# Kernel tuning notes

Hardware: AMD Instinct MI355X
Metric: run time of the kernel (lower is better)

Reference implementation:

```python
import jax, jax.numpy as jnp
import numpy as np

HEAD_NUM = 8
NEG_BIG = 1e9  # additive mask constant from the original layer


def setup_inputs() -> dict:
    key = jax.random.key(0)
    ks = jax.random.split(key, 7)
    B, S, D = 4, 2048, 512
    return {
        "x": jax.random.normal(ks[0], (B, S, D), dtype=jnp.float32),
        "Wk": jax.random.normal(ks[1], (D, D), dtype=jnp.float32) * (1.0 / np.sqrt(D)),
        "bk": jax.random.normal(ks[2], (D,), dtype=jnp.float32) * 0.02,
        "Wv": jax.random.normal(ks[3], (D, D), dtype=jnp.float32) * (1.0 / np.sqrt(D)),
        "bv": jax.random.normal(ks[4], (D,), dtype=jnp.float32) * 0.02,
        "Wo": jax.random.normal(ks[5], (D, D), dtype=jnp.float32) * (1.0 / np.sqrt(D)),
        "bo": jax.random.normal(ks[6], (D,), dtype=jnp.float32) * 0.02,
    }


def reference(x, Wk, bk, Wv, bv, Wo, bo):
    B, S, D = x.shape
    H = HEAD_NUM
    hd = D // H
    # Original layer: query is NOT projected; key/value are.
    q = x
    k = x @ Wk + bk
    v = x @ Wv + bv
    # split heads: [B, H, S, hd]
    qh = q.reshape(B, S, H, hd).transpose(0, 2, 1, 3)
    kh = k.reshape(B, S, H, hd).transpose(0, 2, 1, 3)
    vh = v.reshape(B, S, H, hd).transpose(0, 2, 1, 3)
    # scaled dot-product scores [B, H, S, S] (normalized=True => 1/sqrt(head_dim))
    scale = 1.0 / jnp.sqrt(jnp.asarray(hd, dtype=x.dtype))
    e = jnp.einsum("bhqd,bhkd->bhqk", qh, kh) * scale
    # history_only=True => causal additive mask
    causal = jnp.tril(jnp.ones((S, S), dtype=x.dtype))
    e = e - (1.0 - causal) * NEG_BIG
    a = jax.nn.softmax(e, axis=-1)
    out = jnp.einsum("bhqk,bhkd->bhqd", a, vh)  # [B, H, S, hd]
    out = out.transpose(0, 2, 1, 3).reshape(B, S, D)
    return out @ Wo + bo
```

## Files before the change

kernel.cpp:

```cpp
#include <hip/hip_runtime.h>
#include <stdint.h>
#include <stddef.h>

typedef short bf16x8 __attribute__((ext_vector_type(8)));
typedef float f32x4 __attribute__((ext_vector_type(4)));
typedef int i32x4 __attribute__((ext_vector_type(4)));

#define AS1 __attribute__((address_space(1)))
#define AS3 __attribute__((address_space(3)))

#define KSCALE 0.18033688011112042f

__device__ __forceinline__ unsigned short f2bf(float f) {
    union { float f; uint32_t u; } v; v.f = f;
    return (unsigned short)((v.u + 0x7fffu + ((v.u >> 16) & 1u)) >> 16);
}

__global__ void cvt_f32_bf16(const float* __restrict__ in, unsigned short* __restrict__ out, int n4) {
    int i = blockIdx.x * blockDim.x + threadIdx.x;
    if (i >= n4) return;
    float4 v = reinterpret_cast<const float4*>(in)[i];
    ushort4 o;
    o.x = f2bf(v.x); o.y = f2bf(v.y); o.z = f2bf(v.z); o.w = f2bf(v.w);
    reinterpret_cast<ushort4*>(out)[i] = o;
}

__global__ void wtrans3(const float* __restrict__ Wk, const float* __restrict__ Wv,
                        const float* __restrict__ Wo,
                        unsigned short* __restrict__ WkT, unsigned short* __restrict__ WvT,
                        unsigned short* __restrict__ WoT) {
    __shared__ float tile[32][33];
    const float* W = (blockIdx.z == 0) ? Wk : (blockIdx.z == 1) ? Wv : Wo;
    unsigned short* WT = (blockIdx.z == 0) ? WkT : (blockIdx.z == 1) ? WvT : WoT;
    int bk = blockIdx.x * 32, bn = blockIdx.y * 32;
    int tx = threadIdx.x, ty = threadIdx.y;
#pragma unroll
    for (int r = 0; r < 32; r += 8)
        tile[ty + r][tx] = W[(size_t)(bk + ty + r) * 512 + bn + tx];
    __syncthreads();
#pragma unroll
    for (int r = 0; r < 32; r += 8)
        WT[(size_t)(bn + ty + r) * 512 + bk + tx] = f2bf(tile[tx][ty + r]);
}

template<int EPI>
__global__ __launch_bounds__(256, 2) void gemm64(const unsigned short* __restrict__ A,
                                                 const unsigned short* __restrict__ BT,
                                                 const float* __restrict__ bias,
                                                 void* __restrict__ outp) {
    __shared__ unsigned short lA[64 * 64];
    __shared__ unsigned short lB[128 * 64];
    const int tid = threadIdx.x;
    const int tile_n = blockIdx.x * 128;
    const int tile_m = blockIdx.y * 64;
    const int wid = tid >> 6, lane = tid & 63;
    const int wm = (wid >> 1) * 32, wn = (wid & 1) * 64;
    const int l16 = lane & 15, lg = lane >> 4;

    f32x4 acc[2][4];
#pragma unroll
    for (int i = 0; i < 2; ++i)
#pragma unroll
        for (int j = 0; j < 4; ++j)
            acc[i][j] = (f32x4){0.f, 0.f, 0.f, 0.f};

    const int r0 = tid >> 3;
    const int cr = tid & 7;

    for (int kt = 0; kt < 512; kt += 64) {
#pragma unroll
        for (int i = 0; i < 2; ++i) {
            int r = r0 + i * 32;
            int crs = cr ^ (r & 7);
            __builtin_amdgcn_global_load_lds((const AS1 void*)(A + (size_t)(tile_m + r) * 512 + kt + crs * 8),
                                             (AS3 void*)(&lA[(i * 256 + tid) * 8]), 16, 0, 0);
        }
#pragma unroll
        for (int i = 0; i < 4; ++i) {
            int r = r0 + i * 32;
            int crs = cr ^ (r & 7);
            __builtin_amdgcn_global_load_lds((const AS1 void*)(BT + (size_t)(tile_n + r) * 512 + kt + crs * 8),
                                             (AS3 void*)(&lB[(i * 256 + tid) * 8]), 16, 0, 0);
        }
        __syncthreads();
#pragma unroll
        for (int ks = 0; ks < 2; ++ks) {
            bf16x8 af[2], bfr[4];
#pragma unroll
            for (int f = 0; f < 2; ++f) {
                int ra = wm + f * 16 + l16;
                af[f] = *reinterpret_cast<const bf16x8*>(
                    reinterpret_cast<const char*>(lA) + ra * 128 + (((ks * 4 + lg) ^ (ra & 7)) << 4));
            }
#pragma unroll
            for (int f = 0; f < 4; ++f) {
                int rb = wn + f * 16 + l16;
                bfr[f] = *reinterpret_cast<const bf16x8*>(
                    reinterpret_cast<const char*>(lB) + rb * 128 + (((ks * 4 + lg) ^ (rb & 7)) << 4));
            }
#pragma unroll
            for (int fm = 0; fm < 2; ++fm)
#pragma unroll
                for (int fn = 0; fn < 4; ++fn)
                    acc[fm][fn] = __builtin_amdgcn_mfma_f32_16x16x32_bf16(af[fm], bfr[fn], acc[fm][fn], 0, 0, 0);
        }
        __syncthreads();
    }

#pragma unroll
    for (int fm = 0; fm < 2; ++fm)
#pragma unroll
        for (int fn = 0; fn < 4; ++fn) {
            int gm0 = tile_m + wm + fm * 16 + lg * 4;
            int gn = tile_n + wn + fn * 16 + l16;
            float bs = bias[gn];
#pragma unroll
            for (int r = 0; r < 4; ++r) {
                float v = acc[fm][fn][r] + bs;
                int m = gm0 + r;
                if (EPI == 0) {
                    v *= KSCALE;
                    int b = m >> 11, s = m & 2047, h = gn >> 6, d = gn & 63;
                    ((unsigned short*)outp)[(((size_t)(b * 8 + h) * 2048 + s) << 6) + d] = f2bf(v);
                } else if (EPI == 1) {
                    int b = m >> 11, s = m & 2047, h = gn >> 6, d = gn & 63;
                    ((unsigned short*)outp)[(((size_t)(b * 8 + h) * 64 + d) << 11) + s] = f2bf(v);
                } else {
                    ((float*)outp)[(size_t)m * 512 + gn] = v;
                }
            }
        }
}

__global__ __launch_bounds__(256, 4) void attn_f(const unsigned short* __restrict__ xq,
                                                 const unsigned short* __restrict__ kg,
                                                 const unsigned short* __restrict__ vT,
                                                 unsigned short* __restrict__ ob) {
    __shared__ unsigned short lsK[2][4096];
    __shared__ unsigned short lsV[2][4096];

    const int tid = threadIdx.x;
    const int lane = tid & 63;
    const int w = tid >> 6;
    const int l16 = lane & 15, lg = lane >> 4;
    const int bh = blockIdx.x, b = bh >> 3, h = bh & 7;
    const int qblk = 31 - blockIdx.y;
    const int qlo = qblk * 64 + w * 16;
    const int q = qlo + l16;

    const unsigned short* Kb = kg + (size_t)bh * (2048 * 64);
    const unsigned short* Vb = vT + (size_t)bh * (64 * 2048);

    const unsigned short* qp = xq + ((size_t)(b * 2048 + qlo + l16) * 512) + h * 64 + lg * 8;
    bf16x8 qf0 = *(const bf16x8*)qp;
    bf16x8 qf1 = *(const bf16x8*)(qp + 32);

    f32x4 o[4];
#pragma unroll
    for (int i = 0; i < 4; ++i) o[i] = (f32x4){0.f, 0.f, 0.f, 0.f};
    float lsum = 0.f;

    const int nph = qblk + 1;

    const int srow = tid >> 3;
    const int scs = (tid & 7) ^ (srow & 7);
    const int skey = 8 * ((srow >> 2) & 3) + (srow & 3) + 4 * (srow >> 4);

#define STAGE(B, PH) { \
        const int kv0_ = (PH) << 6; \
        __builtin_amdgcn_global_load_lds((const AS1 void*)(Kb + (size_t)(kv0_ + skey) * 64 + scs * 8), \
            (AS3 void*)(&lsK[B][(size_t)tid * 8]), 16, 0, 0); \
        __builtin_amdgcn_global_load_lds((const AS1 void*)(Kb + (size_t)(kv0_ + 32 + skey) * 64 + scs * 8), \
            (AS3 void*)(&lsK[B][(size_t)(256 + tid) * 8]), 16, 0, 0); \
        __builtin_amdgcn_global_load_lds((const AS1 void*)(Vb + (size_t)srow * 2048 + kv0_ + scs * 8), \
            (AS3 void*)(&lsV[B][(size_t)tid * 8]), 16, 0, 0); \
        __builtin_amdgcn_global_load_lds((const AS1 void*)(Vb + (size_t)(srow + 32) * 2048 + kv0_ + scs * 8), \
            (AS3 void*)(&lsV[B][(size_t)(256 + tid) * 8]), 16, 0, 0); }

#define QKGRP(G, PA, PB, KS, KVB) { \
            const char* r0p = (KS) + (32 * (G) + l16) * 128; \
            const char* r1p = r0p + 16 * 128; \
            bf16x8 k00 = *(const bf16x8*)(r0p + ((lg ^ sw) << 4)); \
            bf16x8 k01 = *(const bf16x8*)(r0p + (((lg + 4) ^ sw) << 4)); \
            bf16x8 k10 = *(const bf16x8*)(r1p + ((lg ^ sw) << 4)); \
            bf16x8 k11 = *(const bf16x8*)(r1p + (((lg + 4) ^ sw) << 4)); \
            f32x4 sA = (f32x4){0.f,0.f,0.f,0.f}, sB = (f32x4){0.f,0.f,0.f,0.f}; \
            __builtin_amdgcn_s_setprio(1); \
            sA = __builtin_amdgcn_mfma_f32_16x16x32_bf16(k00, qf0, sA, 0, 0, 0); \
            sA = __builtin_amdgcn_mfma_f32_16x16x32_bf16(k01, qf1, sA, 0, 0, 0); \
            sB = __builtin_amdgcn_mfma_f32_16x16x32_bf16(k10, qf0, sB, 0, 0, 0); \
            sB = __builtin_amdgcn_mfma_f32_16x16x32_bf16(k11, qf1, sB, 0, 0, 0); \
            __builtin_amdgcn_s_setprio(0); \
            if ((KVB) + 32 * (G) + 31 > qlo) { \
                _Pragma("unroll") \
                for (int r = 0; r < 4; ++r) { \
                    int kidx = (KVB) + 32 * (G) + 8 * lg + r; \
                    PA[r] = __builtin_amdgcn_exp2f(kidx > q ? -1e30f : sA[r]); \
                    PB[r] = __builtin_amdgcn_exp2f(kidx + 4 > q ? -1e30f : sB[r]); \
                } \
            } else { \
                _Pragma("unroll") \
                for (int r = 0; r < 4; ++r) { \
                    PA[r] = __builtin_amdgcn_exp2f(sA[r]); \
                    PB[r] = __builtin_amdgcn_exp2f(sB[r]); \
                } \
            } }

    const int sw = l16 & 7;
    STAGE(0, 0);
    for (int ph = 0; ph < nph; ++ph) {
        const int cur = ph & 1;
        if (ph + 1 < nph) {
            STAGE(cur ^ 1, ph + 1);
            asm volatile("s_waitcnt vmcnt(4)" ::: "memory");
        } else {
            asm volatile("s_waitcnt vmcnt(0)" ::: "memory");
        }
        __builtin_amdgcn_s_barrier();
        asm volatile("" ::: "memory");
        {
            const char* KS = (const char*)lsK[cur];
            const char* VS = (const char*)lsV[cur];
            const int kvb = ph << 6;
            float pA0[4], pB0[4], pA1[4], pB1[4];
            QKGRP(0, pA0, pB0, KS, kvb)
            QKGRP(1, pA1, pB1, KS, kvb)
            lsum += ((pA0[0] + pA0[1]) + (pA0[2] + pA0[3]))
                  + ((pB0[0] + pB0[1]) + (pB0[2] + pB0[3]))
                  + ((pA1[0] + pA1[1]) + (pA1[2] + pA1[3]))
                  + ((pB1[0] + pB1[1]) + (pB1[2] + pB1[3]));
            uint32_t u0, u1, u2, u3, u4, u5, u6, u7;
            asm("v_cvt_pk_bf16_f32 %0, %1, %2" : "=v"(u0) : "v"(pA0[0]), "v"(pA0[1]));
            asm("v_cvt_pk_bf16_f32 %0, %1, %2" : "=v"(u1) : "v"(pA0[2]), "v"(pA0[3]));
            asm("v_cvt_pk_bf16_f32 %0, %1, %2" : "=v"(u2) : "v"(pB0[0]), "v"(pB0[1]));
            asm("v_cvt_pk_bf16_f32 %0, %1, %2" : "=v"(u3) : "v"(pB0[2]), "v"(pB0[3]));
            asm("v_cvt_pk_bf16_f32 %0, %1, %2" : "=v"(u4) : "v"(pA1[0]), "v"(pA1[1]));
            asm("v_cvt_pk_bf16_f32 %0, %1, %2" : "=v"(u5) : "v"(pA1[2]), "v"(pA1[3]));
            asm("v_cvt_pk_bf16_f32 %0, %1, %2" : "=v"(u6) : "v"(pB1[0]), "v"(pB1[1]));
            asm("v_cvt_pk_bf16_f32 %0, %1, %2" : "=v"(u7) : "v"(pB1[2]), "v"(pB1[3]));
            union { i32x4 i; bf16x8 h; } pu0, pu1;
            pu0.i = (i32x4){(int)u0, (int)u1, (int)u2, (int)u3};
            pu1.i = (i32x4){(int)u4, (int)u5, (int)u6, (int)u7};
            __builtin_amdgcn_s_setprio(1);
#pragma unroll
            for (int nb = 0; nb < 4; ++nb) {
                const char* vr = VS + (nb * 16 + l16) * 128;
                bf16x8 vf0 = *(const bf16x8*)(vr + ((lg ^ sw) << 4));
                bf16x8 vf1 = *(const bf16x8*)(vr + (((lg + 4) ^ sw) << 4));
                o[nb] = __builtin_amdgcn_mfma_f32_16x16x32_bf16(pu0.h, vf0, o[nb], 0, 0, 0);
                o[nb] = __builtin_amdgcn_mfma_f32_16x16x32_bf16(pu1.h, vf1, o[nb], 0, 0, 0);
            }
            __builtin_amdgcn_s_setprio(0);
        }
        asm volatile("" ::: "memory");
        __builtin_amdgcn_s_barrier();
    }
#undef STAGE
#undef QKGRP

    lsum += __shfl_xor(lsum, 16, 64);
    lsum += __shfl_xor(lsum, 32, 64);
    float linv[4];
#pragma unroll
    for (int r = 0; r < 4; ++r)
        linv[r] = 1.f / __shfl(lsum, 4 * lg + r, 64);
#pragma unroll
    for (int nb = 0; nb < 4; ++nb)
#pragma unroll
        for (int r = 0; r < 4; ++r) {
            int s = qlo + 4 * lg + r;
            ob[(size_t)(b * 2048 + s) * 512 + h * 64 + nb * 16 + l16] = f2bf(o[nb][r] * linv[r]);
        }
}

extern "C" void kernel_launch(void* const* d_in, const int* in_sizes, int n_in,
                              void* d_out, int out_size, void* d_ws, size_t ws_size,
                              hipStream_t stream) {
    const float* x  = (const float*)d_in[0];
    const float* Wk = (const float*)d_in[1];
    const float* bk = (const float*)d_in[2];
    const float* Wv = (const float*)d_in[3];
    const float* bv = (const float*)d_in[4];
    const float* Wo = (const float*)d_in[5];
    const float* bo = (const float*)d_in[6];

    char* ws = (char*)d_ws;
    unsigned short* xb   = (unsigned short*)(ws);
    unsigned short* kbuf = (unsigned short*)(ws + (8ull << 20));
    unsigned short* vTb  = (unsigned short*)(ws + (16ull << 20));
    unsigned short* obuf = (unsigned short*)(ws + (24ull << 20));
    unsigned short* WkT  = (unsigned short*)(ws + (32ull << 20));
    unsigned short* WvT  = (unsigned short*)(ws + (33ull << 20));
    unsigned short* WoT  = (unsigned short*)(ws + (34ull << 20));

    cvt_f32_bf16<<<4096, 256, 0, stream>>>(x, xb, 1048576);
    wtrans3<<<dim3(16, 16, 3), dim3(32, 8), 0, stream>>>(Wk, Wv, Wo, WkT, WvT, WoT);

    dim3 gg(4, 128);
    gemm64<0><<<gg, 256, 0, stream>>>(xb, WkT, bk, kbuf);
    gemm64<1><<<gg, 256, 0, stream>>>(xb, WvT, bv, vTb);

    attn_f<<<dim3(32, 32), 256, 0, stream>>>(xb, kbuf, vTb, obuf);

    gemm64<2><<<gg, 256, 0, stream>>>(obuf, WoT, bo, d_out);
}
```

Baseline: 79.81 us.

## Fuse K/V projection GEMMs and double query rows per attention wave

The K and V projections become one GEMM launch over a concatenated transposed weight (N=1024), and its epilogue routes each column to the scaled K layout or the transposed V layout. The attention kernel now gives each wave 32 query rows (two 16-row groups) in 128-row blocks, so each staged K/V tile feeds twice as many MFMAs. Query blocks are ordered in a balanced pattern across the 16 y-blocks. This removes one launch and halves K/V LDS traffic per query, but raises register pressure and adds per-group causal activity branches.

```diff
diff --git a/kernel.cpp b/kernel.cpp
--- a/kernel.cpp
+++ b/kernel.cpp
@@ -10,6 +10,7 @@
 #define AS3 __attribute__((address_space(3)))
 
 #define KSCALE 0.18033688011112042f
+#define MFMA16(A, B, C) __builtin_amdgcn_mfma_f32_16x16x32_bf16(A, B, C, 0, 0, 0)
 
 __device__ __forceinline__ unsigned short f2bf(float f) {
     union { float f; uint32_t u; } v; v.f = f;
@@ -27,11 +28,10 @@
 
 __global__ void wtrans3(const float* __restrict__ Wk, const float* __restrict__ Wv,
                         const float* __restrict__ Wo,
-                        unsigned short* __restrict__ WkT, unsigned short* __restrict__ WvT,
-                        unsigned short* __restrict__ WoT) {
+                        unsigned short* __restrict__ WkvT, unsigned short* __restrict__ WoT) {
     __shared__ float tile[32][33];
     const float* W = (blockIdx.z == 0) ? Wk : (blockIdx.z == 1) ? Wv : Wo;
-    unsigned short* WT = (blockIdx.z == 0) ? WkT : (blockIdx.z == 1) ? WvT : WoT;
+    unsigned short* WT = (blockIdx.z == 2) ? WoT : (WkvT + (size_t)blockIdx.z * 512 * 512);
     int bk = blockIdx.x * 32, bn = blockIdx.y * 32;
     int tx = threadIdx.x, ty = threadIdx.y;
 #pragma unroll
@@ -43,11 +43,12 @@
         WT[(size_t)(bn + ty + r) * 512 + bk + tx] = f2bf(tile[tx][ty + r]);
 }
 
-template<int EPI>
-__global__ __launch_bounds__(256, 2) void gemm64(const unsigned short* __restrict__ A,
+__global__ __launch_bounds__(256, 2) void gemmKV(const unsigned short* __restrict__ A,
                                                  const unsigned short* __restrict__ BT,
-                                                 const float* __restrict__ bias,
-                                                 void* __restrict__ outp) {
+                                                 const float* __restrict__ bk,
+                                                 const float* __restrict__ bv,
+                                                 unsigned short* __restrict__ kbuf,
+                                                 unsigned short* __restrict__ vTb) {
     __shared__ unsigned short lA[64 * 64];
     __shared__ unsigned short lB[128 * 64];
     const int tid = threadIdx.x;
@@ -102,7 +103,93 @@
             for (int fm = 0; fm < 2; ++fm)
 #pragma unroll
                 for (int fn = 0; fn < 4; ++fn)
-                    acc[fm][fn] = __builtin_amdgcn_mfma_f32_16x16x32_bf16(af[fm], bfr[fn], acc[fm][fn], 0, 0, 0);
+                    acc[fm][fn] = MFMA16(af[fm], bfr[fn], acc[fm][fn]);
+        }
+        __syncthreads();
+    }
+
+#pragma unroll
+    for (int fm = 0; fm < 2; ++fm)
+#pragma unroll
+        for (int fn = 0; fn < 4; ++fn) {
+            int gm0 = tile_m + wm + fm * 16 + lg * 4;
+            int gn = tile_n + wn + fn * 16 + l16;
+            bool isK = gn < 512;
+            int gnn = isK ? gn : gn - 512;
+            float bs = isK ? bk[gnn] : bv[gnn];
+            int hh = gnn >> 6, d = gnn & 63;
+#pragma unroll
+            for (int r = 0; r < 4; ++r) {
+                float v = acc[fm][fn][r] + bs;
+                int m = gm0 + r;
+                int b = m >> 11, s = m & 2047;
+                if (isK)
+                    kbuf[(((size_t)(b * 8 + hh) * 2048 + s) << 6) + d] = f2bf(v * KSCALE);
+                else
+                    vTb[(((size_t)(b * 8 + hh) * 64 + d) << 11) + s] = f2bf(v);
+            }
+        }
+}
+
+__global__ __launch_bounds__(256, 2) void gemmO(const unsigned short* __restrict__ A,
+                                                const unsigned short* __restrict__ BT,
+                                                const float* __restrict__ bias,
+                                                float* __restrict__ outp) {
+    __shared__ unsigned short lA[64 * 64];
+    __shared__ unsigned short lB[128 * 64];
+    const int tid = threadIdx.x;
+    const int tile_n = blockIdx.x * 128;
+    const int tile_m = blockIdx.y * 64;
+    const int wid = tid >> 6, lane = tid & 63;
+    const int wm = (wid >> 1) * 32, wn = (wid & 1) * 64;
+    const int l16 = lane & 15, lg = lane >> 4;
+
+    f32x4 acc[2][4];
+#pragma unroll
+    for (int i = 0; i < 2; ++i)
+#pragma unroll
+        for (int j = 0; j < 4; ++j)
+            acc[i][j] = (f32x4){0.f, 0.f, 0.f, 0.f};
+
+    const int r0 = tid >> 3;
+    const int cr = tid & 7;
+
+    for (int kt = 0; kt < 512; kt += 64) {
+#pragma unroll
+        for (int i = 0; i < 2; ++i) {
+            int r = r0 + i * 32;
+            int crs = cr ^ (r & 7);
+            __builtin_amdgcn_global_load_lds((const AS1 void*)(A + (size_t)(tile_m + r) * 512 + kt + crs * 8),
+                                             (AS3 void*)(&lA[(i * 256 + tid) * 8]), 16, 0, 0);
+        }
+#pragma unroll
+        for (int i = 0; i < 4; ++i) {
+            int r = r0 + i * 32;
+            int crs = cr ^ (r & 7);
+            __builtin_amdgcn_global_load_lds((const AS1 void*)(BT + (size_t)(tile_n + r) * 512 + kt + crs * 8),
+                                             (AS3 void*)(&lB[(i * 256 + tid) * 8]), 16, 0, 0);
+        }
+        __syncthreads();
+#pragma unroll
+        for (int ks = 0; ks < 2; ++ks) {
+            bf16x8 af[2], bfr[4];
+#pragma unroll
+            for (int f = 0; f < 2; ++f) {
+                int ra = wm + f * 16 + l16;
+                af[f] = *reinterpret_cast<const bf16x8*>(
+                    reinterpret_cast<const char*>(lA) + ra * 128 + (((ks * 4 + lg) ^ (ra & 7)) << 4));
+            }
+#pragma unroll
+            for (int f = 0; f < 4; ++f) {
+                int rb = wn + f * 16 + l16;
+                bfr[f] = *reinterpret_cast<const bf16x8*>(
+                    reinterpret_cast<const char*>(lB) + rb * 128 + (((ks * 4 + lg) ^ (rb & 7)) << 4));
+            }
+#pragma unroll
+            for (int fm = 0; fm < 2; ++fm)
+#pragma unroll
+                for (int fn = 0; fn < 4; ++fn)
+                    acc[fm][fn] = MFMA16(af[fm], bfr[fn], acc[fm][fn]);
         }
         __syncthreads();
     }
@@ -115,20 +202,8 @@
             int gn = tile_n + wn + fn * 16 + l16;
             float bs = bias[gn];
 #pragma unroll
-            for (int r = 0; r < 4; ++r) {
-                float v = acc[fm][fn][r] + bs;
-                int m = gm0 + r;
-                if (EPI == 0) {
-                    v *= KSCALE;
-                    int b = m >> 11, s = m & 2047, h = gn >> 6, d = gn & 63;
-                    ((unsigned short*)outp)[(((size_t)(b * 8 + h) * 2048 + s) << 6) + d] = f2bf(v);
-                } else if (EPI == 1) {
-                    int b = m >> 11, s = m & 2047, h = gn >> 6, d = gn & 63;
-                    ((unsigned short*)outp)[(((size_t)(b * 8 + h) * 64 + d) << 11) + s] = f2bf(v);
-                } else {
-                    ((float*)outp)[(size_t)m * 512 + gn] = v;
-                }
-            }
+            for (int r = 0; r < 4; ++r)
+                outp[(size_t)(gm0 + r) * 512 + gn] = acc[fm][fn][r] + bs;
         }
 }
 
@@ -144,23 +219,28 @@
     const int w = tid >> 6;
     const int l16 = lane & 15, lg = lane >> 4;
     const int bh = blockIdx.x, b = bh >> 3, h = bh & 7;
-    const int qblk = 31 - blockIdx.y;
-    const int qlo = qblk * 64 + w * 16;
-    const int q = qlo + l16;
+    const int y = blockIdx.y;
+    const int qblk = (y < 8) ? (15 - y) : (y - 8);
+    const int qlo = qblk * 128 + w * 32;
+    const int qA = qlo + l16;
 
     const unsigned short* Kb = kg + (size_t)bh * (2048 * 64);
     const unsigned short* Vb = vT + (size_t)bh * (64 * 2048);
 
-    const unsigned short* qp = xq + ((size_t)(b * 2048 + qlo + l16) * 512) + h * 64 + lg * 8;
-    bf16x8 qf0 = *(const bf16x8*)qp;
-    bf16x8 qf1 = *(const bf16x8*)(qp + 32);
-
-    f32x4 o[4];
-#pragma unroll
-    for (int i = 0; i < 4; ++i) o[i] = (f32x4){0.f, 0.f, 0.f, 0.f};
-    float lsum = 0.f;
-
-    const int nph = qblk + 1;
+    const unsigned short* qpA = xq + ((size_t)(b * 2048 + qlo + l16) * 512) + h * 64 + lg * 8;
+    bf16x8 qfA0 = *(const bf16x8*)qpA;
+    bf16x8 qfA1 = *(const bf16x8*)(qpA + 32);
+    bf16x8 qfB0 = *(const bf16x8*)(qpA + 16 * 512);
+    bf16x8 qfB1 = *(const bf16x8*)(qpA + 16 * 512 + 32);
+
+    f32x4 oA[4], oB[4];
+#pragma unroll
+    for (int i = 0; i < 4; ++i) { oA[i] = (f32x4){0.f, 0.f, 0.f, 0.f}; oB[i] = (f32x4){0.f, 0.f, 0.f, 0.f}; }
+    float lsumA = 0.f, lsumB = 0.f;
+
+    const int nph = 2 * qblk + 2;
+    const int myntA = ((qlo + 15) >> 6) + 1;
+    const int myntB = ((qlo + 31) >> 6) + 1;
 
     const int srow = tid >> 3;
     const int scs = (tid & 7) ^ (srow & 7);
@@ -177,34 +257,50 @@
         __builtin_amdgcn_global_load_lds((const AS1 void*)(Vb + (size_t)(srow + 32) * 2048 + kv0_ + scs * 8), \
             (AS3 void*)(&lsV[B][(size_t)(256 + tid) * 8]), 16, 0, 0); }
 
-#define QKGRP(G, PA, PB, KS, KVB) { \
-            const char* r0p = (KS) + (32 * (G) + l16) * 128; \
+#define QK2(G, SA0, SA1, SB0, SB1) { \
+            const char* r0p = KS + (32 * (G) + l16) * 128; \
             const char* r1p = r0p + 16 * 128; \
             bf16x8 k00 = *(const bf16x8*)(r0p + ((lg ^ sw) << 4)); \
             bf16x8 k01 = *(const bf16x8*)(r0p + (((lg + 4) ^ sw) << 4)); \
             bf16x8 k10 = *(const bf16x8*)(r1p + ((lg ^ sw) << 4)); \
             bf16x8 k11 = *(const bf16x8*)(r1p + (((lg + 4) ^ sw) << 4)); \
-            f32x4 sA = (f32x4){0.f,0.f,0.f,0.f}, sB = (f32x4){0.f,0.f,0.f,0.f}; \
             __builtin_amdgcn_s_setprio(1); \
-            sA = __builtin_amdgcn_mfma_f32_16x16x32_bf16(k00, qf0, sA, 0, 0, 0); \
-            sA = __builtin_amdgcn_mfma_f32_16x16x32_bf16(k01, qf1, sA, 0, 0, 0); \
-            sB = __builtin_amdgcn_mfma_f32_16x16x32_bf16(k10, qf0, sB, 0, 0, 0); \
-            sB = __builtin_amdgcn_mfma_f32_16x16x32_bf16(k11, qf1, sB, 0, 0, 0); \
-            __builtin_amdgcn_s_setprio(0); \
-            if ((KVB) + 32 * (G) + 31 > qlo) { \
+            SB0 = MFMA16(k00, qfB0, SB0); SB0 = MFMA16(k01, qfB1, SB0); \
+            SB1 = MFMA16(k10, qfB0, SB1); SB1 = MFMA16(k11, qfB1, SB1); \
+            if (actA) { \
+                SA0 = MFMA16(k00, qfA0, SA0); SA0 = MFMA16(k01, qfA1, SA0); \
+                SA1 = MFMA16(k10, qfA0, SA1); SA1 = MFMA16(k11, qfA1, SA1); \
+            } \
+            __builtin_amdgcn_s_setprio(0); }
+
+#define MEXP(G, S0, S1, P0, P1, QROW, QMIN) { \
+            if (kvb + 32 * (G) + 31 > (QMIN)) { \
                 _Pragma("unroll") \
                 for (int r = 0; r < 4; ++r) { \
-                    int kidx = (KVB) + 32 * (G) + 8 * lg + r; \
-                    PA[r] = __builtin_amdgcn_exp2f(kidx > q ? -1e30f : sA[r]); \
-                    PB[r] = __builtin_amdgcn_exp2f(kidx + 4 > q ? -1e30f : sB[r]); \
+                    int kidx = kvb + 32 * (G) + 8 * lg + r; \
+                    P0[r] = __builtin_amdgcn_exp2f(kidx > (QROW) ? -1e30f : S0[r]); \
+                    P1[r] = __builtin_amdgcn_exp2f(kidx + 4 > (QROW) ? -1e30f : S1[r]); \
                 } \
             } else { \
                 _Pragma("unroll") \
                 for (int r = 0; r < 4; ++r) { \
-                    PA[r] = __builtin_amdgcn_exp2f(sA[r]); \
-                    PB[r] = __builtin_amdgcn_exp2f(sB[r]); \
+                    P0[r] = __builtin_amdgcn_exp2f(S0[r]); \
+                    P1[r] = __builtin_amdgcn_exp2f(S1[r]); \
                 } \
             } }
+
+#define CVT8(P0, P1, P2, P3, PU0, PU1) { \
+            uint32_t u0, u1, u2, u3, u4, u5, u6, u7; \
+            asm("v_cvt_pk_bf16_f32 %0, %1, %2" : "=v"(u0) : "v"(P0[0]), "v"(P0[1])); \
+            asm("v_cvt_pk_bf16_f32 %0, %1, %2" : "=v"(u1) : "v"(P0[2]), "v"(P0[3])); \
+            asm("v_cvt_pk_bf16_f32 %0, %1, %2" : "=v"(u2) : "v"(P1[0]), "v"(P1[1])); \
+            asm("v_cvt_pk_bf16_f32 %0, %1, %2" : "=v"(u3) : "v"(P1[2]), "v"(P1[3])); \
+            asm("v_cvt_pk_bf16_f32 %0, %1, %2" : "=v"(u4) : "v"(P2[0]), "v"(P2[1])); \
+            asm("v_cvt_pk_bf16_f32 %0, %1, %2" : "=v"(u5) : "v"(P2[2]), "v"(P2[3])); \
+            asm("v_cvt_pk_bf16_f32 %0, %1, %2" : "=v"(u6) : "v"(P3[0]), "v"(P3[1])); \
+            asm("v_cvt_pk_bf16_f32 %0, %1, %2" : "=v"(u7) : "v"(P3[2]), "v"(P3[3])); \
+            PU0.i = (i32x4){(int)u0, (int)u1, (int)u2, (int)u3}; \
+            PU1.i = (i32x4){(int)u4, (int)u5, (int)u6, (int)u7}; }
 
     const int sw = l16 & 7;
     STAGE(0, 0);
@@ -218,37 +314,48 @@
         }
         __builtin_amdgcn_s_barrier();
         asm volatile("" ::: "memory");
-        {
+        const bool actA = ph < myntA;
+        const bool actB = ph < myntB;
+        if (actB) {
             const char* KS = (const char*)lsK[cur];
             const char* VS = (const char*)lsV[cur];
             const int kvb = ph << 6;
-            float pA0[4], pB0[4], pA1[4], pB1[4];
-            QKGRP(0, pA0, pB0, KS, kvb)
-            QKGRP(1, pA1, pB1, KS, kvb)
-            lsum += ((pA0[0] + pA0[1]) + (pA0[2] + pA0[3]))
-                  + ((pB0[0] + pB0[1]) + (pB0[2] + pB0[3]))
-                  + ((pA1[0] + pA1[1]) + (pA1[2] + pA1[3]))
-                  + ((pB1[0] + pB1[1]) + (pB1[2] + pB1[3]));
-            uint32_t u0, u1, u2, u3, u4, u5, u6, u7;
-            asm("v_cvt_pk_bf16_f32 %0, %1, %2" : "=v"(u0) : "v"(pA0[0]), "v"(pA0[1]));
-            asm("v_cvt_pk_bf16_f32 %0, %1, %2" : "=v"(u1) : "v"(pA0[2]), "v"(pA0[3]));
-            asm("v_cvt_pk_bf16_f32 %0, %1, %2" : "=v"(u2) : "v"(pB0[0]), "v"(pB0[1]));
-            asm("v_cvt_pk_bf16_f32 %0, %1, %2" : "=v"(u3) : "v"(pB0[2]), "v"(pB0[3]));
-            asm("v_cvt_pk_bf16_f32 %0, %1, %2" : "=v"(u4) : "v"(pA1[0]), "v"(pA1[1]));
-            asm("v_cvt_pk_bf16_f32 %0, %1, %2" : "=v"(u5) : "v"(pA1[2]), "v"(pA1[3]));
-            asm("v_cvt_pk_bf16_f32 %0, %1, %2" : "=v"(u6) : "v"(pB1[0]), "v"(pB1[1]));
-            asm("v_cvt_pk_bf16_f32 %0, %1, %2" : "=v"(u7) : "v"(pB1[2]), "v"(pB1[3]));
-            union { i32x4 i; bf16x8 h; } pu0, pu1;
-            pu0.i = (i32x4){(int)u0, (int)u1, (int)u2, (int)u3};
-            pu1.i = (i32x4){(int)u4, (int)u5, (int)u6, (int)u7};
+            f32x4 sa0 = (f32x4){0.f,0.f,0.f,0.f}, sa1 = sa0, sa2 = sa0, sa3 = sa0;
+            f32x4 sb0 = sa0, sb1 = sa0, sb2 = sa0, sb3 = sa0;
+            QK2(0, sa0, sa1, sb0, sb1)
+            QK2(1, sa2, sa3, sb2, sb3)
+            float pb0[4], pb1[4], pb2[4], pb3[4];
+            MEXP(0, sb0, sb1, pb0, pb1, qA + 16, qlo + 16)
+            MEXP(1, sb2, sb3, pb2, pb3, qA + 16, qlo + 16)
+            lsumB += ((pb0[0] + pb0[1]) + (pb0[2] + pb0[3]))
+                   + ((pb1[0] + pb1[1]) + (pb1[2] + pb1[3]))
+                   + ((pb2[0] + pb2[1]) + (pb2[2] + pb2[3]))
+                   + ((pb3[0] + pb3[1]) + (pb3[2] + pb3[3]));
+            union { i32x4 i; bf16x8 h; } puB0, puB1;
+            CVT8(pb0, pb1, pb2, pb3, puB0, puB1)
+            union { i32x4 i; bf16x8 h; } puA0, puA1;
+            if (actA) {
+                float pa0[4], pa1[4], pa2[4], pa3[4];
+                MEXP(0, sa0, sa1, pa0, pa1, qA, qlo)
+                MEXP(1, sa2, sa3, pa2, pa3, qA, qlo)
+                lsumA += ((pa0[0] + pa0[1]) + (pa0[2] + pa0[3]))
+                       + ((pa1[0] + pa1[1]) + (pa1[2] + pa1[3]))
+                       + ((pa2[0] + pa2[1]) + (pa2[2] + pa2[3]))
+                       + ((pa3[0] + pa3[1]) + (pa3[2] + pa3[3]));
+                CVT8(pa0, pa1, pa2, pa3, puA0, puA1)
+            }
             __builtin_amdgcn_s_setprio(1);
 #pragma unroll
             for (int nb = 0; nb < 4; ++nb) {
                 const char* vr = VS + (nb * 16 + l16) * 128;
                 bf16x8 vf0 = *(const bf16x8*)(vr + ((lg ^ sw) << 4));
                 bf16x8 vf1 = *(const bf16x8*)(vr + (((lg + 4) ^ sw) << 4));
-                o[nb] = __builtin_amdgcn_mfma_f32_16x16x32_bf16(pu0.h, vf0, o[nb], 0, 0, 0);
-                o[nb] = __builtin_amdgcn_mfma_f32_16x16x32_bf16(pu1.h, vf1, o[nb], 0, 0, 0);
+                oB[nb] = MFMA16(puB0.h, vf0, oB[nb]);
+                oB[nb] = MFMA16(puB1.h, vf1, oB[nb]);
+                if (actA) {
+                    oA[nb] = MFMA16(puA0.h, vf0, oA[nb]);
+                    oA[nb] = MFMA16(puA1.h, vf1, oA[nb]);
+                }
             }
             __builtin_amdgcn_s_setprio(0);
         }
@@ -256,20 +363,28 @@
         __builtin_amdgcn_s_barrier();
     }
 #undef STAGE
-#undef QKGRP
-
-    lsum += __shfl_xor(lsum, 16, 64);
-    lsum += __shfl_xor(lsum, 32, 64);
-    float linv[4];
-#pragma unroll
-    for (int r = 0; r < 4; ++r)
-        linv[r] = 1.f / __shfl(lsum, 4 * lg + r, 64);
+#undef QK2
+#undef MEXP
+#undef CVT8
+
+    lsumA += __shfl_xor(lsumA, 16, 64);
+    lsumA += __shfl_xor(lsumA, 32, 64);
+    lsumB += __shfl_xor(lsumB, 16, 64);
+    lsumB += __shfl_xor(lsumB, 32, 64);
+    float linvA[4], linvB[4];
+#pragma unroll
+    for (int r = 0; r < 4; ++r) {
+        linvA[r] = 1.f / __shfl(lsumA, 4 * lg + r, 64);
+        linvB[r] = 1.f / __shfl(lsumB, 4 * lg + r, 64);
+    }
 #pragma unroll
     for (int nb = 0; nb < 4; ++nb)
 #pragma unroll
         for (int r = 0; r < 4; ++r) {
             int s = qlo + 4 * lg + r;
-            ob[(size_t)(b * 2048 + s) * 512 + h * 64 + nb * 16 + l16] = f2bf(o[nb][r] * linv[r]);
+            size_t base = (size_t)(b * 2048 + s) * 512 + h * 64 + nb * 16 + l16;
+            ob[base] = f2bf(oA[nb][r] * linvA[r]);
+            ob[base + 16 * 512] = f2bf(oB[nb][r] * linvB[r]);
         }
 }
 
@@ -285,22 +400,19 @@
     const float* bo = (const float*)d_in[6];
 
     char* ws = (char*)d_ws;
-    unsigned short* xb   = (unsigned short*)(ws);
-    unsigned short* kbuf = (unsigned short*)(ws + (8ull << 20));
-    unsigned short* vTb  = (unsigned short*)(ws + (16ull << 20));
-    unsigned short* obuf = (unsigned short*)(ws + (24ull << 20));
-    unsigned short* WkT  = (unsigned short*)(ws + (32ull << 20));
-    unsigned short* WvT  = (unsigned short*)(ws + (33ull << 20));
-    unsigned short* WoT  = (unsigned short*)(ws + (34ull << 20));
+    unsigned short* xb    = (unsigned short*)(ws);
+    unsigned short* kbuf  = (unsigned short*)(ws + (8ull << 20));
+    unsigned short* vTb   = (unsigned short*)(ws + (16ull << 20));
+    unsigned short* obuf  = (unsigned short*)(ws + (24ull << 20));
+    unsigned short* WkvT  = (unsigned short*)(ws + (32ull << 20));
+    unsigned short* WoT   = (unsigned short*)(ws + (33ull << 20));
 
     cvt_f32_bf16<<<4096, 256, 0, stream>>>(x, xb, 1048576);
-    wtrans3<<<dim3(16, 16, 3), dim3(32, 8), 0, stream>>>(Wk, Wv, Wo, WkT, WvT, WoT);
-
-    dim3 gg(4, 128);
-    gemm64<0><<<gg, 256, 0, stream>>>(xb, WkT, bk, kbuf);
-    gemm64<1><<<gg, 256, 0, stream>>>(xb, WvT, bv, vTb);
-
-    attn_f<<<dim3(32, 32), 256, 0, stream>>>(xb, kbuf, vTb, obuf);
-
-    gemm64<2><<<gg, 256, 0, stream>>>(obuf, WoT, bo, d_out);
-}
+    wtrans3<<<dim3(16, 16, 3), dim3(32, 8), 0, stream>>>(Wk, Wv, Wo, WkvT, WoT);
+
+    gemmKV<<<dim3(8, 128), 256, 0, stream>>>(xb, WkvT, bk, bv, kbuf, vTb);
+
+    attn_f<<<dim3(32, 16), 256, 0, stream>>>(xb, kbuf, vTb, obuf);
+
+    gemmO<<<dim3(4, 128), 256, 0, stream>>>(obuf, WoT, bo, (float*)d_out);
+}
```

Measured after the change: 96.03 us. +20.3%, slower.

## Give each attention wave two 16-row query tiles and compute row sums via MFMA

Applied to the files above, without the earlier changes.

The attention kernel now runs 128 threads per block, and each wave handles 32 query rows as two 16-row fragments. Each K/V fragment loaded from LDS is reused for both, halving LDS reads per unit of MFMA work, and each thread issues eight async global-to-LDS loads per stage. Softmax denominators are accumulated with an MFMA against a ones vector instead of scalar sums plus cross-lane shuffles. Per-fragment causal skipping avoids MFMAs for fully masked tiles. The cost is higher register pressure, fewer waves per block for hiding latency, and summing bf16-rounded probabilities, which slightly changes numerics.

```diff
diff --git a/kernel.cpp b/kernel.cpp
--- a/kernel.cpp
+++ b/kernel.cpp
@@ -10,6 +10,7 @@
 #define AS3 __attribute__((address_space(3)))
 
 #define KSCALE 0.18033688011112042f
+#define MFMA16(A, B, C) __builtin_amdgcn_mfma_f32_16x16x32_bf16(A, B, C, 0, 0, 0)
 
 __device__ __forceinline__ unsigned short f2bf(float f) {
     union { float f; uint32_t u; } v; v.f = f;
@@ -102,7 +103,7 @@
             for (int fm = 0; fm < 2; ++fm)
 #pragma unroll
                 for (int fn = 0; fn < 4; ++fn)
-                    acc[fm][fn] = __builtin_amdgcn_mfma_f32_16x16x32_bf16(af[fm], bfr[fn], acc[fm][fn], 0, 0, 0);
+                    acc[fm][fn] = MFMA16(af[fm], bfr[fn], acc[fm][fn]);
         }
         __syncthreads();
     }
@@ -132,7 +133,7 @@
         }
 }
 
-__global__ __launch_bounds__(256, 4) void attn_f(const unsigned short* __restrict__ xq,
+__global__ __launch_bounds__(128, 2) void attn_f(const unsigned short* __restrict__ xq,
                                                  const unsigned short* __restrict__ kg,
                                                  const unsigned short* __restrict__ vT,
                                                  unsigned short* __restrict__ ob) {
@@ -145,66 +146,90 @@
     const int l16 = lane & 15, lg = lane >> 4;
     const int bh = blockIdx.x, b = bh >> 3, h = bh & 7;
     const int qblk = 31 - blockIdx.y;
-    const int qlo = qblk * 64 + w * 16;
-    const int q = qlo + l16;
+    const int qlo = qblk * 64 + w * 32;
+    const int qA = qlo + l16;
 
     const unsigned short* Kb = kg + (size_t)bh * (2048 * 64);
     const unsigned short* Vb = vT + (size_t)bh * (64 * 2048);
 
     const unsigned short* qp = xq + ((size_t)(b * 2048 + qlo + l16) * 512) + h * 64 + lg * 8;
-    bf16x8 qf0 = *(const bf16x8*)qp;
-    bf16x8 qf1 = *(const bf16x8*)(qp + 32);
-
-    f32x4 o[4];
-#pragma unroll
-    for (int i = 0; i < 4; ++i) o[i] = (f32x4){0.f, 0.f, 0.f, 0.f};
-    float lsum = 0.f;
+    bf16x8 qfA0 = *(const bf16x8*)qp;
+    bf16x8 qfA1 = *(const bf16x8*)(qp + 32);
+    bf16x8 qfB0 = *(const bf16x8*)(qp + 16 * 512);
+    bf16x8 qfB1 = *(const bf16x8*)(qp + 16 * 512 + 32);
+
+    const bf16x8 vones = {(short)0x3F80, (short)0x3F80, (short)0x3F80, (short)0x3F80,
+                          (short)0x3F80, (short)0x3F80, (short)0x3F80, (short)0x3F80};
+
+    f32x4 oA[4], oB[4];
+    f32x4 osA = (f32x4){0.f, 0.f, 0.f, 0.f}, osB = (f32x4){0.f, 0.f, 0.f, 0.f};
+#pragma unroll
+    for (int i = 0; i < 4; ++i) { oA[i] = (f32x4){0.f, 0.f, 0.f, 0.f}; oB[i] = (f32x4){0.f, 0.f, 0.f, 0.f}; }
 
     const int nph = qblk + 1;
-
-    const int srow = tid >> 3;
-    const int scs = (tid & 7) ^ (srow & 7);
-    const int skey = 8 * ((srow >> 2) & 3) + (srow & 3) + 4 * (srow >> 4);
-
+    const int myntA = ((qlo + 15) >> 6) + 1;
+    const int myntB = ((qlo + 31) >> 6) + 1;
+
+    const int s0 = tid >> 3;
+    const int scs = (tid & 7) ^ (s0 & 7);
+    const int sk0 = 8 * (s0 >> 2) + (s0 & 3);
+
+#define GLL(SRC, DST) __builtin_amdgcn_global_load_lds((const AS1 void*)(SRC), (AS3 void*)(DST), 16, 0, 0)
 #define STAGE(B, PH) { \
         const int kv0_ = (PH) << 6; \
-        __builtin_amdgcn_global_load_lds((const AS1 void*)(Kb + (size_t)(kv0_ + skey) * 64 + scs * 8), \
-            (AS3 void*)(&lsK[B][(size_t)tid * 8]), 16, 0, 0); \
-        __builtin_amdgcn_global_load_lds((const AS1 void*)(Kb + (size_t)(kv0_ + 32 + skey) * 64 + scs * 8), \
-            (AS3 void*)(&lsK[B][(size_t)(256 + tid) * 8]), 16, 0, 0); \
-        __builtin_amdgcn_global_load_lds((const AS1 void*)(Vb + (size_t)srow * 2048 + kv0_ + scs * 8), \
-            (AS3 void*)(&lsV[B][(size_t)tid * 8]), 16, 0, 0); \
-        __builtin_amdgcn_global_load_lds((const AS1 void*)(Vb + (size_t)(srow + 32) * 2048 + kv0_ + scs * 8), \
-            (AS3 void*)(&lsV[B][(size_t)(256 + tid) * 8]), 16, 0, 0); }
-
-#define QKGRP(G, PA, PB, KS, KVB) { \
-            const char* r0p = (KS) + (32 * (G) + l16) * 128; \
+        GLL(Kb + (size_t)(kv0_ + sk0     ) * 64 + scs * 8, &lsK[B][(size_t)tid * 8]); \
+        GLL(Kb + (size_t)(kv0_ + sk0 + 4 ) * 64 + scs * 8, &lsK[B][1024 + (size_t)tid * 8]); \
+        GLL(Kb + (size_t)(kv0_ + sk0 + 32) * 64 + scs * 8, &lsK[B][2048 + (size_t)tid * 8]); \
+        GLL(Kb + (size_t)(kv0_ + sk0 + 36) * 64 + scs * 8, &lsK[B][3072 + (size_t)tid * 8]); \
+        GLL(Vb + (size_t)(s0     ) * 2048 + kv0_ + scs * 8, &lsV[B][(size_t)tid * 8]); \
+        GLL(Vb + (size_t)(s0 + 16) * 2048 + kv0_ + scs * 8, &lsV[B][1024 + (size_t)tid * 8]); \
+        GLL(Vb + (size_t)(s0 + 32) * 2048 + kv0_ + scs * 8, &lsV[B][2048 + (size_t)tid * 8]); \
+        GLL(Vb + (size_t)(s0 + 48) * 2048 + kv0_ + scs * 8, &lsV[B][3072 + (size_t)tid * 8]); }
+
+#define QK2(G, SA0, SA1, SB0, SB1) { \
+            const char* r0p = KS + (32 * (G) + l16) * 128; \
             const char* r1p = r0p + 16 * 128; \
             bf16x8 k00 = *(const bf16x8*)(r0p + ((lg ^ sw) << 4)); \
             bf16x8 k01 = *(const bf16x8*)(r0p + (((lg + 4) ^ sw) << 4)); \
             bf16x8 k10 = *(const bf16x8*)(r1p + ((lg ^ sw) << 4)); \
             bf16x8 k11 = *(const bf16x8*)(r1p + (((lg + 4) ^ sw) << 4)); \
-            f32x4 sA = (f32x4){0.f,0.f,0.f,0.f}, sB = (f32x4){0.f,0.f,0.f,0.f}; \
             __builtin_amdgcn_s_setprio(1); \
-            sA = __builtin_amdgcn_mfma_f32_16x16x32_bf16(k00, qf0, sA, 0, 0, 0); \
-            sA = __builtin_amdgcn_mfma_f32_16x16x32_bf16(k01, qf1, sA, 0, 0, 0); \
-            sB = __builtin_amdgcn_mfma_f32_16x16x32_bf16(k10, qf0, sB, 0, 0, 0); \
-            sB = __builtin_amdgcn_mfma_f32_16x16x32_bf16(k11, qf1, sB, 0, 0, 0); \
-            __builtin_amdgcn_s_setprio(0); \
-            if ((KVB) + 32 * (G) + 31 > qlo) { \
+            SB0 = MFMA16(k00, qfB0, SB0); SB0 = MFMA16(k01, qfB1, SB0); \
+            SB1 = MFMA16(k10, qfB0, SB1); SB1 = MFMA16(k11, qfB1, SB1); \
+            if (actA) { \
+                SA0 = MFMA16(k00, qfA0, SA0); SA0 = MFMA16(k01, qfA1, SA0); \
+                SA1 = MFMA16(k10, qfA0, SA1); SA1 = MFMA16(k11, qfA1, SA1); \
+            } \
+            __builtin_amdgcn_s_setprio(0); }
+
+#define MEXP(G, S0, S1, P0, P1, QROW, QMIN) { \
+            if (kvb + 32 * (G) + 31 > (QMIN)) { \
                 _Pragma("unroll") \
                 for (int r = 0; r < 4; ++r) { \
-                    int kidx = (KVB) + 32 * (G) + 8 * lg + r; \
-                    PA[r] = __builtin_amdgcn_exp2f(kidx > q ? -1e30f : sA[r]); \
-                    PB[r] = __builtin_amdgcn_exp2f(kidx + 4 > q ? -1e30f : sB[r]); \
+                    int kidx = kvb + 32 * (G) + 8 * lg + r; \
+                    P0[r] = __builtin_amdgcn_exp2f(kidx > (QROW) ? -1e30f : S0[r]); \
+                    P1[r] = __builtin_amdgcn_exp2f(kidx + 4 > (QROW) ? -1e30f : S1[r]); \
                 } \
             } else { \
                 _Pragma("unroll") \
                 for (int r = 0; r < 4; ++r) { \
-                    PA[r] = __builtin_amdgcn_exp2f(sA[r]); \
-                    PB[r] = __builtin_amdgcn_exp2f(sB[r]); \
+                    P0[r] = __builtin_amdgcn_exp2f(S0[r]); \
+                    P1[r] = __builtin_amdgcn_exp2f(S1[r]); \
                 } \
             } }
+
+#define CVT8(P0, P1, P2, P3, PU0, PU1) { \
+            uint32_t u0, u1, u2, u3, u4, u5, u6, u7; \
+            asm("v_cvt_pk_bf16_f32 %0, %1, %2" : "=v"(u0) : "v"(P0[0]), "v"(P0[1])); \
+            asm("v_cvt_pk_bf16_f32 %0, %1, %2" : "=v"(u1) : "v"(P0[2]), "v"(P0[3])); \
+            asm("v_cvt_pk_bf16_f32 %0, %1, %2" : "=v"(u2) : "v"(P1[0]), "v"(P1[1])); \
+            asm("v_cvt_pk_bf16_f32 %0, %1, %2" : "=v"(u3) : "v"(P1[2]), "v"(P1[3])); \
+            asm("v_cvt_pk_bf16_f32 %0, %1, %2" : "=v"(u4) : "v"(P2[0]), "v"(P2[1])); \
+            asm("v_cvt_pk_bf16_f32 %0, %1, %2" : "=v"(u5) : "v"(P2[2]), "v"(P2[3])); \
+            asm("v_cvt_pk_bf16_f32 %0, %1, %2" : "=v"(u6) : "v"(P3[0]), "v"(P3[1])); \
+            asm("v_cvt_pk_bf16_f32 %0, %1, %2" : "=v"(u7) : "v"(P3[2]), "v"(P3[3])); \
+            PU0.i = (i32x4){(int)u0, (int)u1, (int)u2, (int)u3}; \
+            PU1.i = (i32x4){(int)u4, (int)u5, (int)u6, (int)u7}; }
 
     const int sw = l16 & 7;
     STAGE(0, 0);
@@ -212,43 +237,51 @@
         const int cur = ph & 1;
         if (ph + 1 < nph) {
             STAGE(cur ^ 1, ph + 1);
-            asm volatile("s_waitcnt vmcnt(4)" ::: "memory");
+            asm volatile("s_waitcnt vmcnt(8)" ::: "memory");
         } else {
             asm volatile("s_waitcnt vmcnt(0)" ::: "memory");
         }
         __builtin_amdgcn_s_barrier();
         asm volatile("" ::: "memory");
-        {
+        const bool actA = ph < myntA;
+        if (ph < myntB) {
             const char* KS = (const char*)lsK[cur];
             const char* VS = (const char*)lsV[cur];
             const int kvb = ph << 6;
-            float pA0[4], pB0[4], pA1[4], pB1[4];
-            QKGRP(0, pA0, pB0, KS, kvb)
-            QKGRP(1, pA1, pB1, KS, kvb)
-            lsum += ((pA0[0] + pA0[1]) + (pA0[2] + pA0[3]))
-                  + ((pB0[0] + pB0[1]) + (pB0[2] + pB0[3]))
-                  + ((pA1[0] + pA1[1]) + (pA1[2] + pA1[3]))
-                  + ((pB1[0] + pB1[1]) + (pB1[2] + pB1[3]));
-            uint32_t u0, u1, u2, u3, u4, u5, u6, u7;
-            asm("v_cvt_pk_bf16_f32 %0, %1, %2" : "=v"(u0) : "v"(pA0[0]), "v"(pA0[1]));
-            asm("v_cvt_pk_bf16_f32 %0, %1, %2" : "=v"(u1) : "v"(pA0[2]), "v"(pA0[3]));
-            asm("v_cvt_pk_bf16_f32 %0, %1, %2" : "=v"(u2) : "v"(pB0[0]), "v"(pB0[1]));
-            asm("v_cvt_pk_bf16_f32 %0, %1, %2" : "=v"(u3) : "v"(pB0[2]), "v"(pB0[3]));
-            asm("v_cvt_pk_bf16_f32 %0, %1, %2" : "=v"(u4) : "v"(pA1[0]), "v"(pA1[1]));
-            asm("v_cvt_pk_bf16_f32 %0, %1, %2" : "=v"(u5) : "v"(pA1[2]), "v"(pA1[3]));
-            asm("v_cvt_pk_bf16_f32 %0, %1, %2" : "=v"(u6) : "v"(pB1[0]), "v"(pB1[1]));
-            asm("v_cvt_pk_bf16_f32 %0, %1, %2" : "=v"(u7) : "v"(pB1[2]), "v"(pB1[3]));
-            union { i32x4 i; bf16x8 h; } pu0, pu1;
-            pu0.i = (i32x4){(int)u0, (int)u1, (int)u2, (int)u3};
-            pu1.i = (i32x4){(int)u4, (int)u5, (int)u6, (int)u7};
+            f32x4 sa0 = (f32x4){0.f,0.f,0.f,0.f}, sa1 = sa0, sa2 = sa0, sa3 = sa0;
+            f32x4 sb0 = sa0, sb1 = sa0, sb2 = sa0, sb3 = sa0;
+            QK2(0, sa0, sa1, sb0, sb1)
+            QK2(1, sa2, sa3, sb2, sb3)
+            float pb0[4], pb1[4], pb2[4], pb3[4];
+            MEXP(0, sb0, sb1, pb0, pb1, qA + 16, qlo + 16)
+            MEXP(1, sb2, sb3, pb2, pb3, qA + 16, qlo + 16)
+            union { i32x4 i; bf16x8 h; } puB0, puB1;
+            CVT8(pb0, pb1, pb2, pb3, puB0, puB1)
+            union { i32x4 i; bf16x8 h; } puA0, puA1;
+            if (actA) {
+                float pa0[4], pa1[4], pa2[4], pa3[4];
+                MEXP(0, sa0, sa1, pa0, pa1, qA, qlo)
+                MEXP(1, sa2, sa3, pa2, pa3, qA, qlo)
+                CVT8(pa0, pa1, pa2, pa3, puA0, puA1)
+            }
             __builtin_amdgcn_s_setprio(1);
+            osB = MFMA16(puB0.h, vones, osB);
+            osB = MFMA16(puB1.h, vones, osB);
+            if (actA) {
+                osA = MFMA16(puA0.h, vones, osA);
+                osA = MFMA16(puA1.h, vones, osA);
+            }
 #pragma unroll
             for (int nb = 0; nb < 4; ++nb) {
                 const char* vr = VS + (nb * 16 + l16) * 128;
                 bf16x8 vf0 = *(const bf16x8*)(vr + ((lg ^ sw) << 4));
                 bf16x8 vf1 = *(const bf16x8*)(vr + (((lg + 4) ^ sw) << 4));
-                o[nb] = __builtin_amdgcn_mfma_f32_16x16x32_bf16(pu0.h, vf0, o[nb], 0, 0, 0);
-                o[nb] = __builtin_amdgcn_mfma_f32_16x16x32_bf16(pu1.h, vf1, o[nb], 0, 0, 0);
+                oB[nb] = MFMA16(puB0.h, vf0, oB[nb]);
+                oB[nb] = MFMA16(puB1.h, vf1, oB[nb]);
+                if (actA) {
+                    oA[nb] = MFMA16(puA0.h, vf0, oA[nb]);
+                    oA[nb] = MFMA16(puA1.h, vf1, oA[nb]);
+                }
             }
             __builtin_amdgcn_s_setprio(0);
         }
@@ -256,20 +289,25 @@
         __builtin_amdgcn_s_barrier();
     }
 #undef STAGE
-#undef QKGRP
-
-    lsum += __shfl_xor(lsum, 16, 64);
-    lsum += __shfl_xor(lsum, 32, 64);
-    float linv[4];
-#pragma unroll
-    for (int r = 0; r < 4; ++r)
-        linv[r] = 1.f / __shfl(lsum, 4 * lg + r, 64);
+#undef GLL
+#undef QK2
+#undef MEXP
+#undef CVT8
+
+    float linvA[4], linvB[4];
+#pragma unroll
+    for (int r = 0; r < 4; ++r) {
+        linvA[r] = 1.f / osA[r];
+        linvB[r] = 1.f / osB[r];
+    }
 #pragma unroll
     for (int nb = 0; nb < 4; ++nb)
 #pragma unroll
         for (int r = 0; r < 4; ++r) {
             int s = qlo + 4 * lg + r;
-            ob[(size_t)(b * 2048 + s) * 512 + h * 64 + nb * 16 + l16] = f2bf(o[nb][r] * linv[r]);
+            size_t base = (size_t)(b * 2048 + s) * 512 + h * 64 + nb * 16 + l16;
+            ob[base] = f2bf(oA[nb][r] * linvA[r]);
+            ob[base + 16 * 512] = f2bf(oB[nb][r] * linvB[r]);
         }
 }
 
@@ -300,7 +338,7 @@
     gemm64<0><<<gg, 256, 0, stream>>>(xb, WkT, bk, kbuf);
     gemm64<1><<<gg, 256, 0, stream>>>(xb, WvT, bv, vTb);
 
-    attn_f<<<dim3(32, 32), 256, 0, stream>>>(xb, kbuf, vTb, obuf);
-
-    gemm64<2><<<gg, 256, 0, stream>>>(obuf, WoT, bo, d_out);
-}
+    attn_f<<<dim3(32, 32), 128, 0, stream>>>(xb, kbuf, vTb, obuf);
+
+    gemm64<2><<<gg, 256, 0, stream>>>(obuf, WoT, bo, (float*)d_out);
+}
```

Result: slower. 88.52 us (+10.9%).
